# Kernel optimization log

Hardware: AMD Instinct MI355X
Metric: run time of the kernel (lower is better)

## Reference

```python
import jax, jax.numpy as jnp
import numpy as np

B, S, D, L, V, H, FF = 128, 256, 512, 4, 96, 8, 512
DH = D // H
EPS = 1e-3  # keras BatchNormalization default epsilon


def setup_inputs() -> dict:
    key = jax.random.key(0)
    ks = jax.random.split(key, 12)
    s = 0.02
    inp = {
        "sequence": jax.random.randint(ks[0], (B, S), 0, V),
        "pos_encodings": jax.random.normal(ks[1], (S, D), jnp.float32) * s,
        "embed": jax.random.normal(ks[2], (V, D), jnp.float32) * s,
        "Wq": jax.random.normal(ks[3], (L, D, D), jnp.float32) * s,
        "bq": jnp.zeros((L, D), jnp.float32),
        "Wk": jax.random.normal(ks[4], (L, D, D), jnp.float32) * s,
        "bk": jnp.zeros((L, D), jnp.float32),
        "Wv": jax.random.normal(ks[5], (L, D, D), jnp.float32) * s,
        "bv": jnp.zeros((L, D), jnp.float32),
        "Wo": jax.random.normal(ks[6], (L, D, D), jnp.float32) * s,
        "bo": jnp.zeros((L, D), jnp.float32),
        "gamma1": jnp.ones((L, D), jnp.float32),
        "beta1": jnp.zeros((L, D), jnp.float32),
        "W1": jax.random.normal(ks[7], (L, D, FF), jnp.float32) * s,
        "b1": jnp.zeros((L, FF), jnp.float32),
        "W2": jax.random.normal(ks[8], (L, FF, D), jnp.float32) * s,
        "b2": jnp.zeros((L, D), jnp.float32),
        "gamma2": jnp.ones((L, D), jnp.float32),
        "beta2": jnp.zeros((L, D), jnp.float32),
    }
    return inp


def _batchnorm(h, g, b):
    # training-mode BN over (batch, seq) per feature, eps=1e-3
    mu = jnp.mean(h, axis=(0, 1), keepdims=True)
    var = jnp.mean(jnp.square(h - mu), axis=(0, 1), keepdims=True)
    return (h - mu) * jax.lax.rsqrt(var + EPS) * g + b


def _encoder(sequence, pos_encodings, embed, layer_params):
    x = embed[sequence] + pos_encodings[None]  # [B,S,D]

    def layer(h, p):
        wq, bq_, wk, bk_, wv, bv_, wo, bo_, g1, be1, w1, bb1, w2, bb2, g2, be2 = p
        b_, s_, d_ = h.shape
        q = (h @ wq + bq_).reshape(b_, s_, H, DH)
        k = (h @ wk + bk_).reshape(b_, s_, H, DH)
        v = (h @ wv + bv_).reshape(b_, s_, H, DH)
        scores = jnp.einsum('bqhd,bkhd->bhqk', q, k) / jnp.sqrt(jnp.float32(DH))
        attn = jnp.einsum('bhqk,bkhd->bqhd', jax.nn.softmax(scores, axis=-1), v)
        attn = attn.reshape(b_, s_, d_) @ wo + bo_
        h = _batchnorm(h + attn, g1, be1)
        ffn = jax.nn.relu(h @ w1 + bb1) @ w2 + bb2
        h = _batchnorm(h + ffn, g2, be2)
        return h, None

    out, _ = jax.lax.scan(layer, x, layer_params)
    return out


def reference(sequence, pos_encodings, embed, Wq, bq, Wk, bk, Wv, bv, Wo, bo,
              gamma1, beta1, W1, b1, W2, b2, gamma2, beta2):
    layer_params = (Wq, bq, Wk, bk, Wv, bv, Wo, bo,
                    gamma1, beta1, W1, b1, W2, b2, gamma2, beta2)
    return _encoder(sequence, pos_encodings, embed, layer_params)
```

## Files before the change

### kernel.cpp

```cpp
#include <hip/hip_runtime.h>

#define B_   128
#define S_   256
#define D_   512
#define L_   4
#define H_   8
#define DH_  64
#define FF_  512
#define M_   32768
#define EPS_ 1e-3f

typedef unsigned short u16;
typedef unsigned int   u32;
typedef __bf16 bf16_8 __attribute__((ext_vector_type(8)));
typedef float  f32_4  __attribute__((ext_vector_type(4)));

__device__ __forceinline__ float bf2f(u16 u) {
  union { u32 i; float f; } x; x.i = ((u32)u) << 16; return x.f;
}
__device__ __forceinline__ u16 f2bf(float f) {
  union { float f; u32 i; } x; x.f = f;
  u32 r = x.i + 0x7fffu + ((x.i >> 16) & 1u);
  return (u16)(r >> 16);
}
__device__ __forceinline__ void async_cp16(const void* g, void* l) {
  __builtin_amdgcn_global_load_lds(
      (const __attribute__((address_space(1))) void*)g,
      (__attribute__((address_space(3))) void*)l, 16, 0, 0);
}

__global__ __launch_bounds__(256) void k_embed(const int* __restrict__ seq,
    const float* __restrict__ pos, const float* __restrict__ emb,
    u16* __restrict__ h)
{
  int t = blockIdx.x * 256 + threadIdx.x;
  int row = t >> 6;
  int c = (t & 63) * 8;
  int s = row & (S_ - 1);
  int tok = seq[row];
  const float* ep = emb + (size_t)tok * D_ + c;
  const float* pp = pos + (size_t)s * D_ + c;
  float4 e0 = *(const float4*)ep;
  float4 e1 = *(const float4*)(ep + 4);
  float4 p0 = *(const float4*)pp;
  float4 p1 = *(const float4*)(pp + 4);
  u32 o[4];
  o[0] = (u32)f2bf(e0.x + p0.x) | ((u32)f2bf(e0.y + p0.y) << 16);
  o[1] = (u32)f2bf(e0.z + p0.z) | ((u32)f2bf(e0.w + p0.w) << 16);
  o[2] = (u32)f2bf(e1.x + p1.x) | ((u32)f2bf(e1.y + p1.y) << 16);
  o[3] = (u32)f2bf(e1.z + p1.z) | ((u32)f2bf(e1.w + p1.w) << 16);
  *(uint4*)&h[(size_t)row * D_ + c] = make_uint4(o[0], o[1], o[2], o[3]);
}

__global__ __launch_bounds__(256) void k_transpose(
    const float* __restrict__ Wq, const float* __restrict__ Wk, const float* __restrict__ Wv,
    const float* __restrict__ Wo, const float* __restrict__ W1, const float* __restrict__ W2,
    u16* __restrict__ Wt)
{
  __shared__ u16 tile[32][33];
  int mat = blockIdx.z;
  int layer = mat / 6, w = mat % 6;
  const float* src = (w == 0) ? Wq : (w == 1) ? Wk : (w == 2) ? Wv
                   : (w == 3) ? Wo : (w == 4) ? W1 : W2;
  src += (size_t)layer * (D_ * D_);
  u16* dst = Wt + (size_t)mat * (D_ * D_);
  int bx = blockIdx.x * 32;
  int by = blockIdx.y * 32;
  int tx = threadIdx.x & 31, ty = threadIdx.x >> 5;
#pragma unroll
  for (int i = 0; i < 32; i += 8)
    tile[ty + i][tx] = f2bf(src[(size_t)(by + ty + i) * D_ + bx + tx]);
  __syncthreads();
#pragma unroll
  for (int i = 0; i < 32; i += 8)
    dst[(size_t)(bx + ty + i) * D_ + by + tx] = tile[tx][ty + i];
}

__global__ __launch_bounds__(256) void k_packbias(const float* __restrict__ bq,
    const float* __restrict__ bk, const float* __restrict__ bv, float* __restrict__ dst)
{
  int t = blockIdx.x * 256 + threadIdx.x;
  int l = t / 1536, j = t - l * 1536;
  const float* src = (j < 512) ? bq : (j < 1024) ? bk : bv;
  dst[t] = src[l * 512 + (j & 511)];
}

__global__ __launch_bounds__(256) void k_gemm(
    const u16* __restrict__ A, const u16* __restrict__ Bt,
    const float* __restrict__ bias, const u16* __restrict__ resid,
    u16* __restrict__ outb, float* __restrict__ outf, float* __restrict__ stats,
    int mode)
{
  __shared__ u16 As[3 * 128 * 32];
  __shared__ u16 Bs[3 * 128 * 32];
  int tid = threadIdx.x;
  int m0 = blockIdx.x * 128;
  int n0 = blockIdx.y * 128;
  int w = tid >> 6, lane = tid & 63;
  int wm = (w >> 1) * 64, wn = (w & 1) * 64;
  int fr = lane & 15, lk = lane >> 4;

  int srow = lane >> 2;
  int schunk = (lane & 3) ^ ((lane >> 4) & 3);
  const u16* Ag0 = A  + (size_t)(m0 + w * 32 + srow) * 512 + schunk * 8;
  const u16* Ag1 = Ag0 + (size_t)16 * 512;
  const u16* Bg0 = Bt + (size_t)(n0 + w * 32 + srow) * 512 + schunk * 8;
  const u16* Bg1 = Bg0 + (size_t)16 * 512;
  int off0 = (w * 32) * 32;
  int off1 = (w * 32 + 16) * 32;

  f32_4 acc[4][4] = {};
  int ach = (lk ^ ((fr >> 2) & 3)) * 8;

  async_cp16(Ag0, &As[off0]);
  async_cp16(Ag1, &As[off1]);
  async_cp16(Bg0, &Bs[off0]);
  async_cp16(Bg1, &Bs[off1]);
  async_cp16(Ag0 + 32, &As[4096 + off0]);
  async_cp16(Ag1 + 32, &As[4096 + off1]);
  async_cp16(Bg0 + 32, &Bs[4096 + off0]);
  async_cp16(Bg1 + 32, &Bs[4096 + off1]);

#pragma unroll
  for (int it = 0; it < 16; it++) {
    if (it < 15) asm volatile("s_waitcnt vmcnt(4)" ::: "memory");
    else         asm volatile("s_waitcnt vmcnt(0)" ::: "memory");
    __builtin_amdgcn_s_barrier();
    asm volatile("" ::: "memory");
    if (it < 14) {
      int kn = (it + 2) * 32;
      int pn = ((it + 2) % 3) * 4096;
      async_cp16(Ag0 + kn, &As[pn + off0]);
      async_cp16(Ag1 + kn, &As[pn + off1]);
      async_cp16(Bg0 + kn, &Bs[pn + off0]);
      async_cp16(Bg1 + kn, &Bs[pn + off1]);
    }
    const u16* Ab = &As[(it % 3) * 4096];
    const u16* Bb = &Bs[(it % 3) * 4096];
    bf16_8 afr[4], bfr[4];
#pragma unroll
    for (int i = 0; i < 4; i++) {
      afr[i] = *(const bf16_8*)&Ab[(wm + i * 16 + fr) * 32 + ach];
      bfr[i] = *(const bf16_8*)&Bb[(wn + i * 16 + fr) * 32 + ach];
    }
#pragma unroll
    for (int i = 0; i < 4; i++)
#pragma unroll
      for (int j = 0; j < 4; j++)
        acc[i][j] = __builtin_amdgcn_mfma_f32_16x16x32_bf16(afr[i], bfr[j], acc[i][j], 0, 0, 0);
  }

  int rbase = lk * 4;
#pragma unroll
  for (int j = 0; j < 4; j++) {
    int col = n0 + wn + j * 16 + fr;
    float bv = bias[col];
    float csum = 0.f, csq = 0.f;
#pragma unroll
    for (int i = 0; i < 4; i++) {
      int row = m0 + wm + i * 16 + rbase;
#pragma unroll
      for (int r = 0; r < 4; r++) {
        float c = acc[i][j][r] + bv;
        if (mode == 1) c = fmaxf(c, 0.f);
        if (mode == 2) {
          size_t idx = (size_t)(row + r) * 512 + col;
          c += bf2f(resid[idx]);
          outf[idx] = c;
          csum += c; csq = fmaf(c, c, csq);
        } else if (mode == 3) {
          int rr = row + r;
          int cc = col & 511;
          size_t idx = (size_t)(col >> 9) * ((size_t)M_ * D_)
                     + ((size_t)((rr >> 8) * 8 + (cc >> 6)) * 256 + (rr & 255)) * 64 + (cc & 63);
          outb[idx] = f2bf(c);
        } else {
          outb[(size_t)(row + r) * 512 + col] = f2bf(c);
        }
      }
    }
    if (mode == 2) {
      csum += __shfl_xor(csum, 16); csum += __shfl_xor(csum, 32);
      csq  += __shfl_xor(csq, 16);  csq  += __shfl_xor(csq, 32);
      if (lk == 0) {
        atomicAdd(&stats[col], csum);
        atomicAdd(&stats[512 + col], csq);
      }
    }
  }
}

__global__ __launch_bounds__(256) void k_attn(
    const u16* __restrict__ q, const u16* __restrict__ k,
    const u16* __restrict__ v, u16* __restrict__ attn)
{
  __shared__ u16 Vt[64 * 256];
  __shared__ u16 Pm[4][16 * 64];
  int tid = threadIdx.x;
  int h = blockIdx.x & 7, b = blockIdx.x >> 3;
  size_t hb = (size_t)(b * 8 + h) * (256 * 64);
  int w = tid >> 6, lane = tid & 63;

  {
    int kp = tid & 127;
    int o  = tid >> 7;
    const u16* vp = v + hb + (size_t)(2 * kp) * 64 + o * 32;
    union { uint4 u[4]; u16 s[32]; } r0, r1;
#pragma unroll
    for (int i = 0; i < 4; i++) {
      r0.u[i] = *(const uint4*)(vp + i * 8);
      r1.u[i] = *(const uint4*)(vp + 64 + i * 8);
    }
#pragma unroll
    for (int d = 0; d < 32; d++) {
      int da = o * 32 + d;
      u32 val = (u32)r0.s[d] | ((u32)r1.s[d] << 16);
      int idx = da * 256 + ((((kp >> 2) ^ (da & 31)) << 3)) + ((2 * kp) & 7);
      *(u32*)&Vt[idx] = val;
    }
  }
  __syncthreads();

  int fr = lane & 15;
  int lk = lane >> 4;
  int rbase = lk * 4;
  const u16* kb = k + hb;

#pragma unroll 1
  for (int qt = 0; qt < 4; qt++) {
    int q0 = qt * 64 + w * 16;

    f32_4 accS[16];
    const u16* qbase = q + hb + (size_t)(q0 + fr) * 64 + lk * 8;
    bf16_8 af0 = *(const bf16_8*)(qbase);
    bf16_8 af1 = *(const bf16_8*)(qbase + 32);
#pragma unroll
    for (int j = 0; j < 16; j++) {
      const u16* kr = kb + (size_t)(j * 16 + fr) * 64;
      bf16_8 bf0 = *(const bf16_8*)(kr + lk * 8);
      bf16_8 bf1 = *(const bf16_8*)(kr + 32 + lk * 8);
      f32_4 z = {};
      z = __builtin_amdgcn_mfma_f32_16x16x32_bf16(af0, bf0, z, 0, 0, 0);
      accS[j] = __builtin_amdgcn_mfma_f32_16x16x32_bf16(af1, bf1, z, 0, 0, 0);
    }

    float l[4];
#pragma unroll
    for (int r = 0; r < 4; r++) {
      float m = accS[0][r];
#pragma unroll
      for (int j = 1; j < 16; j++) m = fmaxf(m, accS[j][r]);
      m = fmaxf(m, __shfl_xor(m, 1));
      m = fmaxf(m, __shfl_xor(m, 2));
      m = fmaxf(m, __shfl_xor(m, 4));
      m = fmaxf(m, __shfl_xor(m, 8));
      float s = 0.f;
#pragma unroll
      for (int j = 0; j < 16; j++) {
        float p = __expf((accS[j][r] - m) * 0.125f);
        accS[j][r] = p;
        s += p;
      }
      s += __shfl_xor(s, 1);
      s += __shfl_xor(s, 2);
      s += __shfl_xor(s, 4);
      s += __shfl_xor(s, 8);
      l[r] = s;
    }

    f32_4 accO[4] = {};
#pragma unroll
    for (int hs = 0; hs < 4; hs++) {
#pragma unroll
      for (int j4 = 0; j4 < 4; j4++) {
        int col = j4 * 16 + fr;
        int ch = col >> 3, cl = col & 7;
#pragma unroll
        for (int r = 0; r < 4; r++) {
          int row = rbase + r;
          Pm[w][row * 64 + ((ch ^ (row & 7)) << 3) + cl] = f2bf(accS[hs * 4 + j4][r]);
        }
      }
#pragma unroll
      for (int kk = 0; kk < 2; kk++) {
        bf16_8 pa = *(const bf16_8*)&Pm[w][fr * 64 + (((kk * 4 + lk) ^ (fr & 7)) << 3)];
#pragma unroll
        for (int jd = 0; jd < 4; jd++) {
          int brow = jd * 16 + fr;
          int ck = hs * 8 + kk * 4 + lk;
          bf16_8 vb = *(const bf16_8*)&Vt[brow * 256 + ((ck ^ (brow & 31)) << 3)];
          accO[jd] = __builtin_amdgcn_mfma_f32_16x16x32_bf16(pa, vb, accO[jd], 0, 0, 0);
        }
      }
    }

    float linv[4];
#pragma unroll
    for (int r = 0; r < 4; r++) linv[r] = 1.f / l[r];
    size_t orow0 = (size_t)(b * S_ + q0 + rbase);
#pragma unroll
    for (int jd = 0; jd < 4; jd++) {
      int col = h * DH_ + jd * 16 + fr;
#pragma unroll
      for (int r = 0; r < 4; r++)
        attn[(orow0 + r) * D_ + col] = f2bf(accO[jd][r] * linv[r]);
    }
  }
}

__global__ __launch_bounds__(256) void k_zero(float* p, int n) {
  int t = blockIdx.x * 256 + threadIdx.x;
  if (t < n) p[t] = 0.f;
}

__global__ __launch_bounds__(256) void k_bnapply(const float* __restrict__ P,
    const float* __restrict__ stats, const float* __restrict__ gamma,
    const float* __restrict__ beta, u16* __restrict__ outb, float* __restrict__ outf)
{
  size_t t8 = ((size_t)blockIdx.x * 256 + threadIdx.x) * 8;
  int f = (int)(t8 & 511);
  const float inv = 1.f / 32768.f;
  float sc[8], sh[8];
#pragma unroll
  for (int i = 0; i < 8; i++) {
    float mu = stats[f + i] * inv;
    float var = stats[512 + f + i] * inv - mu * mu;
    sc[i] = gamma[f + i] * rsqrtf(var + EPS_);
    sh[i] = beta[f + i] - mu * sc[i];
  }
  float4 p0 = *(const float4*)&P[t8];
  float4 p1 = *(const float4*)&P[t8 + 4];
  float o[8] = {p0.x * sc[0] + sh[0], p0.y * sc[1] + sh[1],
                p0.z * sc[2] + sh[2], p0.w * sc[3] + sh[3],
                p1.x * sc[4] + sh[4], p1.y * sc[5] + sh[5],
                p1.z * sc[6] + sh[6], p1.w * sc[7] + sh[7]};
  if (outf) {
    *(float4*)&outf[t8]     = make_float4(o[0], o[1], o[2], o[3]);
    *(float4*)&outf[t8 + 4] = make_float4(o[4], o[5], o[6], o[7]);
  } else {
    u32 u[4];
#pragma unroll
    for (int i = 0; i < 4; i++)
      u[i] = (u32)f2bf(o[2 * i]) | ((u32)f2bf(o[2 * i + 1]) << 16);
    *(uint4*)&outb[t8] = make_uint4(u[0], u[1], u[2], u[3]);
  }
}

extern "C" void kernel_launch(void* const* d_in, const int* in_sizes, int n_in,
                              void* d_out, int out_size, void* d_ws, size_t ws_size,
                              hipStream_t stream)
{
  const int*   seq = (const int*)d_in[0];
  const float* pos = (const float*)d_in[1];
  const float* emb = (const float*)d_in[2];
  const float* Wq  = (const float*)d_in[3];
  const float* bq  = (const float*)d_in[4];
  const float* Wk  = (const float*)d_in[5];
  const float* bk  = (const float*)d_in[6];
  const float* Wv  = (const float*)d_in[7];
  const float* bv  = (const float*)d_in[8];
  const float* Wo  = (const float*)d_in[9];
  const float* bo  = (const float*)d_in[10];
  const float* g1  = (const float*)d_in[11];
  const float* be1 = (const float*)d_in[12];
  const float* W1  = (const float*)d_in[13];
  const float* b1  = (const float*)d_in[14];
  const float* W2  = (const float*)d_in[15];
  const float* b2  = (const float*)d_in[16];
  const float* g2  = (const float*)d_in[17];
  const float* be2 = (const float*)d_in[18];

  char* ws = (char*)d_ws;
  const size_t SZH = (size_t)M_ * D_ * 2;
  u16* hb16 = (u16*)(ws);
  u16* qB   = (u16*)(ws + SZH);
  u16* kB   = (u16*)(ws + 2 * SZH);
  u16* vB   = (u16*)(ws + 3 * SZH);
  u16* aB   = (u16*)(ws + 4 * SZH);
  float* PB = (float*)(ws + 2 * SZH);
  u16* tB   = qB;
  u16* Wt   = (u16*)(ws + 5 * SZH);
  float* stats = (float*)(ws + 5 * SZH + (size_t)24 * D_ * D_ * 2);
  float* bqkv  = stats + 8192;

  dim3 blk(256);
  k_zero<<<32, blk, 0, stream>>>(stats, 8192);
  k_packbias<<<24, blk, 0, stream>>>(bq, bk, bv, bqkv);
  k_transpose<<<dim3(16, 16, 24), blk, 0, stream>>>(Wq, Wk, Wv, Wo, W1, W2, Wt);
  k_embed<<<M_ * 64 / 256, blk, 0, stream>>>(seq, pos, emb, hb16);

  dim3 ggrid(M_ / 128, 512 / 128);
  dim3 qgrid(M_ / 128, 1536 / 128);
  for (int l = 0; l < L_; l++) {
    const u16* wtqkv = Wt + (size_t)(l * 6 + 0) * D_ * D_;
    const u16* wto = Wt + (size_t)(l * 6 + 3) * D_ * D_;
    const u16* wt1 = Wt + (size_t)(l * 6 + 4) * D_ * D_;
    const u16* wt2 = Wt + (size_t)(l * 6 + 5) * D_ * D_;
    float* st = stats + l * 2048;

    k_gemm<<<qgrid, blk, 0, stream>>>(hb16, wtqkv, bqkv + l * 1536, nullptr, qB, nullptr, nullptr, 3);
    k_attn<<<B_ * H_, blk, 0, stream>>>(qB, kB, vB, aB);
    k_gemm<<<ggrid, blk, 0, stream>>>(aB, wto, bo + l * D_, hb16, nullptr, PB, st, 2);
    k_bnapply<<<8192, blk, 0, stream>>>(PB, st, g1 + l * D_, be1 + l * D_, hb16, nullptr);
    k_gemm<<<ggrid, blk, 0, stream>>>(hb16, wt1, b1 + l * FF_, nullptr, tB, nullptr, nullptr, 1);
    k_gemm<<<ggrid, blk, 0, stream>>>(tB, wt2, b2 + l * D_, hb16, nullptr, PB, st + 1024, 2);
    if (l == L_ - 1)
      k_bnapply<<<8192, blk, 0, stream>>>(PB, st + 1024, g2 + l * D_, be2 + l * D_, nullptr, (float*)d_out);
    else
      k_bnapply<<<8192, blk, 0, stream>>>(PB, st + 1024, g2 + l * D_, be2 + l * D_, hb16, nullptr);
  }
}
```

Measured before the change: 1.803 ms.

## Stage GEMM epilogue through LDS for vectorized stores; store pre-BN residual as bf16

The GEMM epilogue now writes the bias-added, activated results as bf16 into a swizzled shared-memory tile, then each thread issues coalesced 16-byte global stores, including for the head-major QKV layout. Before, each element went out as a scattered 2-byte store. The pre-BatchNorm residual sum is now kept in bf16 instead of fp32, which halves the write and read traffic between the GEMM and the BN-apply kernel. In exchange, the epilogue needs an extra sync and an LDS round trip. BN normalisation now reads bf16-rounded values while the statistics are still taken from fp32, which may cost some accuracy.

```diff
diff --git a/kernel.cpp b/kernel.cpp
--- a/kernel.cpp
+++ b/kernel.cpp
@@ -88,11 +88,12 @@
 __global__ __launch_bounds__(256) void k_gemm(
     const u16* __restrict__ A, const u16* __restrict__ Bt,
     const float* __restrict__ bias, const u16* __restrict__ resid,
-    u16* __restrict__ outb, float* __restrict__ outf, float* __restrict__ stats,
+    u16* __restrict__ outb, float* __restrict__ stats,
     int mode)
 {
-  __shared__ u16 As[3 * 128 * 32];
-  __shared__ u16 Bs[3 * 128 * 32];
+  __shared__ __align__(16) u16 smem[24576];
+  u16* As = smem;
+  u16* Bs = smem + 12288;
   int tid = threadIdx.x;
   int m0 = blockIdx.x * 128;
   int n0 = blockIdx.y * 128;
@@ -150,42 +151,56 @@
         acc[i][j] = __builtin_amdgcn_mfma_f32_16x16x32_bf16(afr[i], bfr[j], acc[i][j], 0, 0, 0);
   }
 
+  __syncthreads();
+  u16* Ct = smem;
   int rbase = lk * 4;
 #pragma unroll
   for (int j = 0; j < 4; j++) {
-    int col = n0 + wn + j * 16 + fr;
-    float bv = bias[col];
+    int colin = wn + j * 16 + fr;
+    int colg  = n0 + colin;
+    float bv = bias[colg];
     float csum = 0.f, csq = 0.f;
 #pragma unroll
     for (int i = 0; i < 4; i++) {
-      int row = m0 + wm + i * 16 + rbase;
+      int rowl = wm + i * 16 + rbase;
 #pragma unroll
       for (int r = 0; r < 4; r++) {
         float c = acc[i][j][r] + bv;
         if (mode == 1) c = fmaxf(c, 0.f);
         if (mode == 2) {
-          size_t idx = (size_t)(row + r) * 512 + col;
-          c += bf2f(resid[idx]);
-          outf[idx] = c;
+          c += bf2f(resid[(size_t)(m0 + rowl + r) * 512 + colg]);
           csum += c; csq = fmaf(c, c, csq);
-        } else if (mode == 3) {
-          int rr = row + r;
-          int cc = col & 511;
-          size_t idx = (size_t)(col >> 9) * ((size_t)M_ * D_)
-                     + ((size_t)((rr >> 8) * 8 + (cc >> 6)) * 256 + (rr & 255)) * 64 + (cc & 63);
-          outb[idx] = f2bf(c);
-        } else {
-          outb[(size_t)(row + r) * 512 + col] = f2bf(c);
         }
+        int rw = rowl + r;
+        Ct[rw * 128 + (((colin >> 3) ^ (rw & 15)) << 3) + (colin & 7)] = f2bf(c);
       }
     }
     if (mode == 2) {
       csum += __shfl_xor(csum, 16); csum += __shfl_xor(csum, 32);
       csq  += __shfl_xor(csq, 16);  csq  += __shfl_xor(csq, 32);
       if (lk == 0) {
-        atomicAdd(&stats[col], csum);
-        atomicAdd(&stats[512 + col], csq);
+        atomicAdd(&stats[colg], csum);
+        atomicAdd(&stats[512 + colg], csq);
       }
+    }
+  }
+  __syncthreads();
+
+#pragma unroll
+  for (int rd = 0; rd < 8; rd++) {
+    int lrow = w * 32 + rd * 4 + (lane >> 4);
+    int s = lane & 15;
+    uint4 val = *(const uint4*)&Ct[lrow * 128 + s * 8];
+    int chunk = s ^ (lrow & 15);
+    int grow = m0 + lrow;
+    if (mode == 3) {
+      int colg = n0 + chunk * 8;
+      int cc = colg & 511;
+      size_t idx = (size_t)(colg >> 9) * ((size_t)M_ * D_)
+                 + ((size_t)((grow >> 8) * 8 + (cc >> 6)) * 256 + (grow & 255)) * 64 + (cc & 63);
+      *(uint4*)&outb[idx] = val;
+    } else {
+      *(uint4*)&outb[(size_t)grow * 512 + n0 + chunk * 8] = val;
     }
   }
 }
@@ -313,7 +328,7 @@
   if (t < n) p[t] = 0.f;
 }
 
-__global__ __launch_bounds__(256) void k_bnapply(const float* __restrict__ P,
+__global__ __launch_bounds__(256) void k_bnapply(const u16* __restrict__ P,
     const float* __restrict__ stats, const float* __restrict__ gamma,
     const float* __restrict__ beta, u16* __restrict__ outb, float* __restrict__ outf)
 {
@@ -328,12 +343,11 @@
     sc[i] = gamma[f + i] * rsqrtf(var + EPS_);
     sh[i] = beta[f + i] - mu * sc[i];
   }
-  float4 p0 = *(const float4*)&P[t8];
-  float4 p1 = *(const float4*)&P[t8 + 4];
-  float o[8] = {p0.x * sc[0] + sh[0], p0.y * sc[1] + sh[1],
-                p0.z * sc[2] + sh[2], p0.w * sc[3] + sh[3],
-                p1.x * sc[4] + sh[4], p1.y * sc[5] + sh[5],
-                p1.z * sc[6] + sh[6], p1.w * sc[7] + sh[7]};
+  union { uint4 u; u16 s[8]; } pv;
+  pv.u = *(const uint4*)&P[t8];
+  float o[8];
+#pragma unroll
+  for (int i = 0; i < 8; i++) o[i] = bf2f(pv.s[i]) * sc[i] + sh[i];
   if (outf) {
     *(float4*)&outf[t8]     = make_float4(o[0], o[1], o[2], o[3]);
     *(float4*)&outf[t8 + 4] = make_float4(o[4], o[5], o[6], o[7]);
@@ -377,7 +391,7 @@
   u16* kB   = (u16*)(ws + 2 * SZH);
   u16* vB   = (u16*)(ws + 3 * SZH);
   u16* aB   = (u16*)(ws + 4 * SZH);
-  float* PB = (float*)(ws + 2 * SZH);
+  u16* PB   = (u16*)(ws + 2 * SZH);
   u16* tB   = qB;
   u16* Wt   = (u16*)(ws + 5 * SZH);
   float* stats = (float*)(ws + 5 * SZH + (size_t)24 * D_ * D_ * 2);
@@ -398,12 +412,12 @@
     const u16* wt2 = Wt + (size_t)(l * 6 + 5) * D_ * D_;
     float* st = stats + l * 2048;
 
-    k_gemm<<<qgrid, blk, 0, stream>>>(hb16, wtqkv, bqkv + l * 1536, nullptr, qB, nullptr, nullptr, 3);
+    k_gemm<<<qgrid, blk, 0, stream>>>(hb16, wtqkv, bqkv + l * 1536, nullptr, qB, nullptr, 3);
     k_attn<<<B_ * H_, blk, 0, stream>>>(qB, kB, vB, aB);
-    k_gemm<<<ggrid, blk, 0, stream>>>(aB, wto, bo + l * D_, hb16, nullptr, PB, st, 2);
+    k_gemm<<<ggrid, blk, 0, stream>>>(aB, wto, bo + l * D_, hb16, PB, st, 2);
     k_bnapply<<<8192, blk, 0, stream>>>(PB, st, g1 + l * D_, be1 + l * D_, hb16, nullptr);
-    k_gemm<<<ggrid, blk, 0, stream>>>(hb16, wt1, b1 + l * FF_, nullptr, tB, nullptr, nullptr, 1);
-    k_gemm<<<ggrid, blk, 0, stream>>>(tB, wt2, b2 + l * D_, hb16, nullptr, PB, st + 1024, 2);
+    k_gemm<<<ggrid, blk, 0, stream>>>(hb16, wt1, b1 + l * FF_, nullptr, tB, nullptr, 1);
+    k_gemm<<<ggrid, blk, 0, stream>>>(tB, wt2, b2 + l * D_, hb16, PB, st + 1024, 2);
     if (l == L_ - 1)
       k_bnapply<<<8192, blk, 0, stream>>>(PB, st + 1024, g2 + l * D_, be2 + l * D_, nullptr, (float*)d_out);
     else
```

Result: faster. 1.561 ms (-13.5%).
